# Kernel tuning notes

Hardware: AMD Instinct MI355X
Metric: run time of the kernel (lower is better)

The kernel has to match this reference:

```python
import jax, jax.numpy as jnp
import numpy as np

NUM_ROUTING = 3


def squash(t, axis=-1):
    # scale * t / ||t||, scale = ||t||^2 / (1 + ||t||^2)  (matches torch code exactly)
    norm = jnp.sum(t * t, axis=axis, keepdims=True)
    return (norm / (1.0 + norm)) * t / jnp.sqrt(norm)


def setup_inputs() -> dict:
    key = jax.random.key(0)
    k1, k2 = jax.random.split(key)
    x = jax.random.normal(k1, (512, 8, 1152), dtype=jnp.float32)      # [B, in_unit, in_channel]
    W = jax.random.normal(k2, (1, 1152, 10, 16, 8), dtype=jnp.float32)  # [1, C, U, unit_size, in_unit]
    return {"x": x, "W": W}


def reference(x, W):
    B = x.shape[0]
    # x.transpose(1,2): [B, C, I];  u_hat = W @ x  -> [B, C, U, O]  (O = unit_size)
    xt = jnp.transpose(x, (0, 2, 1))
    u_hat = jnp.einsum('cuoi,bci->bcuo', W[0], xt)
    # routing logits b_ij, shared across batch: [C, U]
    b = jnp.zeros(u_hat.shape[1:3], dtype=u_hat.dtype)
    v = None
    for _ in range(NUM_ROUTING):
        c = jax.nn.softmax(b, axis=1)                       # softmax over num_unit dim
        s = jnp.einsum('cu,bcuo->buo', c, u_hat)            # sum over in_channel
        v = squash(s, axis=-1)                              # squash over unit_size
        agree = jnp.einsum('bcuo,buo->cu', u_hat, v) / B    # mean over batch
        b = b + agree
    # torch returns v_j.squeeze(1) with trailing singleton -> [B, U, O, 1]
    return v[..., None]
```

## Files before the change

kernel.cpp:

```cpp
#include <hip/hip_runtime.h>
#include <math.h>

#define B_ 512
#define C_ 1152
#define U_ 10
#define O_ 16
#define I_ 8
#define K_ 9216
#define UO_ 160
#define NBLK 256
#define NTHR 256

typedef short bf16x8 __attribute__((ext_vector_type(8)));
typedef float f32x4 __attribute__((ext_vector_type(4)));
typedef unsigned short u16x8v __attribute__((ext_vector_type(8)));
typedef unsigned long long u64t;

__device__ __attribute__((aligned(16))) unsigned short g_xb2[B_*K_];
__device__ __attribute__((aligned(16))) unsigned short g_xT2[K_*B_];
__device__ __attribute__((aligned(16))) unsigned short g_Wc[3][C_*1280];
__device__ __attribute__((aligned(16))) unsigned g_vT32[2][UO_*B_/2];
__device__ float g_b[C_*U_];
__device__ unsigned g_gen;
__device__ unsigned g_arrive[NBLK];

__device__ __forceinline__ unsigned short f2bf(float f) {
    unsigned u = __builtin_bit_cast(unsigned, f);
    unsigned r = (u + 0x7FFFu + ((u >> 16) & 1u)) >> 16;
    return (unsigned short)r;
}

__device__ __forceinline__ void st_sys16(unsigned short* p, u16x8v v) {
    union { u16x8v v; u64t q[2]; } u; u.v = v;
    __hip_atomic_store((u64t*)p,     u.q[0], __ATOMIC_RELAXED, __HIP_MEMORY_SCOPE_SYSTEM);
    __hip_atomic_store(((u64t*)p)+1, u.q[1], __ATOMIC_RELAXED, __HIP_MEMORY_SCOPE_SYSTEM);
}

__global__ __launch_bounds__(256) void k_prep(const float* __restrict__ x,
                                              const float* __restrict__ W) {
    __shared__ unsigned short lds[32*256];
    int task = blockIdx.x, tid = threadIdx.x;
    if (task < 576) {
        int b0 = (task & 15) * 32;
        int c0 = (task >> 4) * 32;
        int li = tid >> 5, lc = tid & 31;
        for (int rep = 0; rep < 32; rep++) {
            float v = x[(b0+rep)*K_ + li*1152 + c0 + lc];
            lds[rep*256 + ((lc*8+li) ^ ((rep&31)<<3))] = f2bf(v);
        }
        __syncthreads();
        {
            int b = tid >> 3, part = tid & 7;
            int swz = (b&31) << 3;
            const u16x8v* lv = (const u16x8v*)lds;
            u16x8v* ov = (u16x8v*)(g_xb2 + (b0+b)*K_ + c0*8 + part*32);
            #pragma unroll
            for (int g = 0; g < 4; g++)
                ov[g] = lv[(b*256 + ((part*32 + g*8) ^ swz)) >> 3];
        }
        for (int p = 0; p < 8; p++) {
            int r = p*32 + (tid>>3);
            int bp = (tid&7)*4;
            ushort4 o;
            unsigned short* po = (unsigned short*)&o;
            #pragma unroll
            for (int q = 0; q < 4; q++) {
                int b = bp + q;
                po[q] = lds[b*256 + (r ^ ((b&31)<<3))];
            }
            *(ushort4*)(g_xT2 + (c0*8 + r)*B_ + b0 + bp) = o;
        }
    } else {
        int base = (task - 576) * 8192;
        for (int j = 0; j < 8; j++) {
            float4 v = *(const float4*)(W + base + j*1024 + tid*4);
            ushort4 o;
            o.x = f2bf(0.1f*v.x); o.y = f2bf(0.1f*v.y);
            o.z = f2bf(0.1f*v.z); o.w = f2bf(0.1f*v.w);
            *(ushort4*)(&g_Wc[0][0] + base + j*1024 + tid*4) = o;
        }
    }
}

union ShMem {
    float red[4][16][32];
    struct { float agg[2][U_]; float cws[2][U_]; } tb;
};

__device__ __forceinline__ void gbar(unsigned target) {
    __syncthreads();
    if (threadIdx.x == 0)
        __hip_atomic_store(&g_arrive[blockIdx.x], target,
                           __ATOMIC_RELAXED, __HIP_MEMORY_SCOPE_SYSTEM);
    if (blockIdx.x == 0) {
        long spins = 0;
        for (;;) {
            unsigned a = __hip_atomic_load(&g_arrive[threadIdx.x],
                                           __ATOMIC_RELAXED, __HIP_MEMORY_SCOPE_SYSTEM);
            if (__syncthreads_count((int)(a - target) >= 0) == NTHR) break;
            __builtin_amdgcn_s_sleep(4);
            if (++spins > (1L << 17)) break;
        }
        if (threadIdx.x == 0)
            __hip_atomic_store(&g_gen, target, __ATOMIC_RELAXED, __HIP_MEMORY_SCOPE_SYSTEM);
    }
    if (threadIdx.x == 0) {
        long spins = 0;
        while ((int)(__hip_atomic_load(&g_gen, __ATOMIC_RELAXED, __HIP_MEMORY_SCOPE_SYSTEM) - target) < 0) {
            __builtin_amdgcn_s_sleep(8);
            if (++spins > (1L << 18)) break;
        }
    }
    __syncthreads();
}

__device__ void ph_s(const unsigned short* __restrict__ Wcr, unsigned* vtw,
                     float* __restrict__ out, int bid, int tid, ShMem& sh) {
    if (bid < 160) {
        int lane = tid & 63, w = tid >> 6;
        int mt = bid & 31, nt = bid >> 5;
        int m0 = mt*16, n0 = nt*32;
        int ra = lane & 15, kq = (lane>>4)*8;
        const unsigned short* pa  = g_xb2 + (m0+ra)*K_ + w*2304 + kq;
        const unsigned short* pb0 = Wcr + (w*288 + (kq>>3))*1280 + (n0+ra)*8;
        const unsigned short* pb1 = pb0 + 128;
        f32x4 acc0 = {0.f,0.f,0.f,0.f};
        f32x4 acc1 = {0.f,0.f,0.f,0.f};
        #pragma unroll 6
        for (int s = 0; s < 72; s++) {
            bf16x8 a  = *(const bf16x8*)pa;
            bf16x8 b0 = *(const bf16x8*)pb0;
            bf16x8 b1 = *(const bf16x8*)pb1;
            acc0 = __builtin_amdgcn_mfma_f32_16x16x32_bf16(a, b0, acc0, 0, 0, 0);
            acc1 = __builtin_amdgcn_mfma_f32_16x16x32_bf16(a, b1, acc1, 0, 0, 0);
            pa += 32; pb0 += 5120; pb1 += 5120;
        }
        int row = (lane>>4)*4, col = lane & 15;
        #pragma unroll
        for (int r = 0; r < 4; r++) {
            sh.red[w][row+r][col]    = acc0[r];
            sh.red[w][row+r][col+16] = acc1[r];
        }
        __syncthreads();
        int bp = tid >> 5;
        int u  = (tid >> 4) & 1;
        int o  = tid & 15;
        int col2 = u*16 + o;
        float t0 = sh.red[0][2*bp][col2] + sh.red[1][2*bp][col2] + sh.red[2][2*bp][col2] + sh.red[3][2*bp][col2];
        float t1 = sh.red[0][2*bp+1][col2] + sh.red[1][2*bp+1][col2] + sh.red[2][2*bp+1][col2] + sh.red[3][2*bp+1][col2];
        float n0s = t0*t0, n1s = t1*t1;
        #pragma unroll
        for (int m = 1; m < 16; m <<= 1) {
            n0s += __shfl_xor(n0s, m);
            n1s += __shfl_xor(n1s, m);
        }
        float f0 = n0s / ((1.f + n0s) * sqrtf(n0s));
        float f1 = n1s / ((1.f + n1s) * sqrtf(n1s));
        float v0 = t0*f0, v1 = t1*f1;
        int ug = nt*2 + u;
        int bg = m0 + 2*bp;
        if (vtw) {
            unsigned pack = (unsigned)f2bf(v0) | ((unsigned)f2bf(v1) << 16);
            __hip_atomic_store(&vtw[((ug*16+o)*B_ + bg) >> 1], pack,
                               __ATOMIC_RELAXED, __HIP_MEMORY_SCOPE_SYSTEM);
        } else {
            out[(bg*10 + ug)*16 + o]       = v0;
            out[((bg+1)*10 + ug)*16 + o]   = v1;
        }
        __syncthreads();
    }
}

__device__ void ph_tb(const float* __restrict__ W, const unsigned* vtr,
                      unsigned short* Wcw, int first, int bid, int tid, ShMem& sh) {
    int lane = tid & 63, w = tid >> 6;
    const unsigned short* vT = (const unsigned short*)vtr;
    for (int task = bid; task < 576; task += NBLK) {
        int c0 = task * 2;
        int ra = lane & 15, kq = (lane>>4)*8;
        int ct = lane >> 5;
        int i0 = ((lane>>4) & 1) * 4;
        int o  = lane & 15;
        const unsigned short* pa0 = g_xT2 + (c0*8 + ra)*B_ + kq;
        for (int nt = w; nt < 5; nt += 4) {
            int n0 = nt*32;
            const unsigned short* pa  = pa0;
            const unsigned short* pb0 = vT + (n0+ra)*B_ + kq;
            const unsigned short* pb1 = pb0 + 16*B_;
            f32x4 acc0 = {0.f,0.f,0.f,0.f};
            f32x4 acc1 = {0.f,0.f,0.f,0.f};
            #pragma unroll 4
            for (int s = 0; s < 16; s++) {
                bf16x8 a  = *(const bf16x8*)pa;
                bf16x8 b0 = *(const bf16x8*)pb0;
                bf16x8 b1 = *(const bf16x8*)pb1;
                acc0 = __builtin_amdgcn_mfma_f32_16x16x32_bf16(a, b0, acc0, 0, 0, 0);
                acc1 = __builtin_amdgcn_mfma_f32_16x16x32_bf16(a, b1, acc1, 0, 0, 0);
                pa += 32; pb0 += 32; pb1 += 32;
            }
            const float* wr = W + (c0+ct)*1280;
            float4 wa = *(const float4*)(wr + (2*nt  )*128 + o*8 + i0);
            float4 wb = *(const float4*)(wr + (2*nt+1)*128 + o*8 + i0);
            float p0 = wa.x*acc0[0] + wa.y*acc0[1] + wa.z*acc0[2] + wa.w*acc0[3];
            float p1 = wb.x*acc1[0] + wb.y*acc1[1] + wb.z*acc1[2] + wb.w*acc1[3];
            #pragma unroll
            for (int m = 1; m < 32; m <<= 1) {
                p0 += __shfl_xor(p0, m);
                p1 += __shfl_xor(p1, m);
            }
            if ((lane & 31) == 0) {
                sh.tb.agg[ct][2*nt]   = p0 * (1.f/512.f);
                sh.tb.agg[ct][2*nt+1] = p1 * (1.f/512.f);
            }
        }
        __syncthreads();
        if (tid < 2) {
            int c = c0 + tid;
            float bv[U_];
            float mx = -3e38f;
            #pragma unroll
            for (int u = 0; u < U_; u++) {
                float v = sh.tb.agg[tid][u];
                if (!first) v += g_b[c*U_ + u];
                g_b[c*U_ + u] = v;
                bv[u] = v;
                mx = fmaxf(mx, v);
            }
            float sm = 0.f;
            #pragma unroll
            for (int u = 0; u < U_; u++) { bv[u] = expf(bv[u] - mx); sm += bv[u]; }
            float inv = 1.f/sm;
            #pragma unroll
            for (int u = 0; u < U_; u++) sh.tb.cws[tid][u] = bv[u]*inv;
        }
        __syncthreads();
        for (int e = tid*8; e < 2560; e += NTHR*8) {
            int ch  = (e >= 1280) ? 1 : 0;
            int off = e - ch*1280;
            int u   = off >> 7;
            float s = sh.tb.cws[ch][u];
            const float* wp = W + (c0+ch)*1280 + off;
            float4 a4 = *(const float4*)wp;
            float4 b4 = *(const float4*)(wp + 4);
            u16x8v ov;
            ov[0] = f2bf(a4.x*s); ov[1] = f2bf(a4.y*s); ov[2] = f2bf(a4.z*s); ov[3] = f2bf(a4.w*s);
            ov[4] = f2bf(b4.x*s); ov[5] = f2bf(b4.y*s); ov[6] = f2bf(b4.z*s); ov[7] = f2bf(b4.w*s);
            st_sys16(Wcw + (c0+ch)*1280 + off, ov);
        }
        __syncthreads();
    }
}

__global__ __launch_bounds__(NTHR) void k_mega(const float* __restrict__ W,
                                               float* __restrict__ out) {
    __shared__ ShMem sh;
    __shared__ unsigned sG0;
    int bid = blockIdx.x, tid = threadIdx.x;
    if (tid == 0)
        sG0 = __hip_atomic_load(&g_gen, __ATOMIC_RELAXED, __HIP_MEMORY_SCOPE_SYSTEM);
    __syncthreads();
    unsigned G0 = sG0;
    ph_s(&g_Wc[0][0], &g_vT32[0][0], out, bid, tid, sh);
    gbar(G0 + 1);
    ph_tb(W, &g_vT32[0][0], &g_Wc[1][0], 1, bid, tid, sh);
    gbar(G0 + 2);
    ph_s(&g_Wc[1][0], &g_vT32[1][0], out, bid, tid, sh);
    gbar(G0 + 3);
    ph_tb(W, &g_vT32[1][0], &g_Wc[2][0], 0, bid, tid, sh);
    gbar(G0 + 4);
    ph_s(&g_Wc[2][0], nullptr, out, bid, tid, sh);
}

extern "C" void kernel_launch(void* const* d_in, const int* in_sizes, int n_in,
                              void* d_out, int out_size, void* d_ws, size_t ws_size,
                              hipStream_t stream) {
    const float* x = (const float*)d_in[0];
    const float* W = (const float*)d_in[1];
    float* out = (float*)d_out;
    k_prep<<<dim3(756), dim3(256), 0, stream>>>(x, W);
    k_mega<<<dim3(NBLK), dim3(NTHR), 0, stream>>>(W, out);
}
```

Baseline: 145.3 us.

## Quadruple block size to split GEMM K across 16 waves and batch routing tasks

Raises threads per block from 256 to 1024 in the persistent megakernel. The s-phase GEMM now splits the K reduction across 16 waves instead of 4, giving each wave 18 MFMA steps instead of 72 and reducing the partial sums in a larger LDS array. The routing phase runs up to four channel-pair tasks at once per block, one per 256-thread group, instead of looping over them. This aims to shorten the serial latency chains and raise occupancy, at the cost of a wider LDS reduction, larger block-wide barriers, and idle threads in the squash epilogue. The grid barrier is also adjusted so only the first 256 threads poll arrival flags.

After: 123.9 us. 14.7% less time.

```diff
diff --git a/kernel.cpp b/kernel.cpp
--- a/kernel.cpp
+++ b/kernel.cpp
@@ -9,7 +9,7 @@
 #define K_ 9216
 #define UO_ 160
 #define NBLK 256
-#define NTHR 256
+#define NTHR 1024
 
 typedef short bf16x8 __attribute__((ext_vector_type(8)));
 typedef float f32x4 __attribute__((ext_vector_type(4)));
@@ -82,9 +82,10 @@
     }
 }
 
+struct TBsh { float agg[2][U_]; float cws[2][U_]; };
 union ShMem {
-    float red[4][16][32];
-    struct { float agg[2][U_]; float cws[2][U_]; } tb;
+    float red[16][16][32];
+    TBsh tb[4];
 };
 
 __device__ __forceinline__ void gbar(unsigned target) {
@@ -95,9 +96,13 @@
     if (blockIdx.x == 0) {
         long spins = 0;
         for (;;) {
-            unsigned a = __hip_atomic_load(&g_arrive[threadIdx.x],
-                                           __ATOMIC_RELAXED, __HIP_MEMORY_SCOPE_SYSTEM);
-            if (__syncthreads_count((int)(a - target) >= 0) == NTHR) break;
+            int ok = 1;
+            if (threadIdx.x < NBLK) {
+                unsigned a = __hip_atomic_load(&g_arrive[threadIdx.x],
+                                               __ATOMIC_RELAXED, __HIP_MEMORY_SCOPE_SYSTEM);
+                ok = (int)(a - target) >= 0;
+            }
+            if (__syncthreads_count(ok) == NTHR) break;
             __builtin_amdgcn_s_sleep(4);
             if (++spins > (1L << 17)) break;
         }
@@ -120,14 +125,14 @@
         int lane = tid & 63, w = tid >> 6;
         int mt = bid & 31, nt = bid >> 5;
         int m0 = mt*16, n0 = nt*32;
-        int ra = lane & 15, kq = (lane>>4)*8;
-        const unsigned short* pa  = g_xb2 + (m0+ra)*K_ + w*2304 + kq;
-        const unsigned short* pb0 = Wcr + (w*288 + (kq>>3))*1280 + (n0+ra)*8;
+        int ra = lane & 15;
+        const unsigned short* pa  = g_xb2 + (m0+ra)*K_ + w*576 + (lane>>4)*8;
+        const unsigned short* pb0 = Wcr + (w*72 + (lane>>4))*1280 + (n0+ra)*8;
         const unsigned short* pb1 = pb0 + 128;
         f32x4 acc0 = {0.f,0.f,0.f,0.f};
         f32x4 acc1 = {0.f,0.f,0.f,0.f};
         #pragma unroll 6
-        for (int s = 0; s < 72; s++) {
+        for (int s = 0; s < 18; s++) {
             bf16x8 a  = *(const bf16x8*)pa;
             bf16x8 b0 = *(const bf16x8*)pb0;
             bf16x8 b1 = *(const bf16x8*)pb1;
@@ -142,30 +147,36 @@
             sh.red[w][row+r][col+16] = acc1[r];
         }
         __syncthreads();
-        int bp = tid >> 5;
-        int u  = (tid >> 4) & 1;
-        int o  = tid & 15;
-        int col2 = u*16 + o;
-        float t0 = sh.red[0][2*bp][col2] + sh.red[1][2*bp][col2] + sh.red[2][2*bp][col2] + sh.red[3][2*bp][col2];
-        float t1 = sh.red[0][2*bp+1][col2] + sh.red[1][2*bp+1][col2] + sh.red[2][2*bp+1][col2] + sh.red[3][2*bp+1][col2];
-        float n0s = t0*t0, n1s = t1*t1;
-        #pragma unroll
-        for (int m = 1; m < 16; m <<= 1) {
-            n0s += __shfl_xor(n0s, m);
-            n1s += __shfl_xor(n1s, m);
-        }
-        float f0 = n0s / ((1.f + n0s) * sqrtf(n0s));
-        float f1 = n1s / ((1.f + n1s) * sqrtf(n1s));
-        float v0 = t0*f0, v1 = t1*f1;
-        int ug = nt*2 + u;
-        int bg = m0 + 2*bp;
-        if (vtw) {
-            unsigned pack = (unsigned)f2bf(v0) | ((unsigned)f2bf(v1) << 16);
-            __hip_atomic_store(&vtw[((ug*16+o)*B_ + bg) >> 1], pack,
-                               __ATOMIC_RELAXED, __HIP_MEMORY_SCOPE_SYSTEM);
-        } else {
-            out[(bg*10 + ug)*16 + o]       = v0;
-            out[((bg+1)*10 + ug)*16 + o]   = v1;
+        if (tid < 256) {
+            int bp = tid >> 5;
+            int u  = (tid >> 4) & 1;
+            int o  = tid & 15;
+            int col2 = u*16 + o;
+            float t0 = 0.f, t1 = 0.f;
+            #pragma unroll
+            for (int ww = 0; ww < 16; ww++) {
+                t0 += sh.red[ww][2*bp][col2];
+                t1 += sh.red[ww][2*bp+1][col2];
+            }
+            float n0s = t0*t0, n1s = t1*t1;
+            #pragma unroll
+            for (int m = 1; m < 16; m <<= 1) {
+                n0s += __shfl_xor(n0s, m);
+                n1s += __shfl_xor(n1s, m);
+            }
+            float f0 = n0s / ((1.f + n0s) * sqrtf(n0s));
+            float f1 = n1s / ((1.f + n1s) * sqrtf(n1s));
+            float v0 = t0*f0, v1 = t1*f1;
+            int ug = nt*2 + u;
+            int bg = m0 + 2*bp;
+            if (vtw) {
+                unsigned pack = (unsigned)f2bf(v0) | ((unsigned)f2bf(v1) << 16);
+                __hip_atomic_store(&vtw[((ug*16+o)*B_ + bg) >> 1], pack,
+                                   __ATOMIC_RELAXED, __HIP_MEMORY_SCOPE_SYSTEM);
+            } else {
+                out[(bg*10 + ug)*16 + o]       = v0;
+                out[((bg+1)*10 + ug)*16 + o]   = v1;
+            }
         }
         __syncthreads();
     }
@@ -173,16 +184,19 @@
 
 __device__ void ph_tb(const float* __restrict__ W, const unsigned* vtr,
                       unsigned short* Wcw, int first, int bid, int tid, ShMem& sh) {
-    int lane = tid & 63, w = tid >> 6;
+    int lane = tid & 63, lw = (tid >> 6) & 3, g = tid >> 8;
+    int ltid = tid & 255;
+    int t = bid + 256*g;
+    int valid = (t < 576);
     const unsigned short* vT = (const unsigned short*)vtr;
-    for (int task = bid; task < 576; task += NBLK) {
-        int c0 = task * 2;
-        int ra = lane & 15, kq = (lane>>4)*8;
-        int ct = lane >> 5;
-        int i0 = ((lane>>4) & 1) * 4;
-        int o  = lane & 15;
+    int c0 = t * 2;
+    int ra = lane & 15, kq = (lane>>4)*8;
+    int ct = lane >> 5;
+    int i0 = ((lane>>4) & 1) * 4;
+    int o  = lane & 15;
+    if (valid) {
         const unsigned short* pa0 = g_xT2 + (c0*8 + ra)*B_ + kq;
-        for (int nt = w; nt < 5; nt += 4) {
+        for (int nt = lw; nt < 5; nt += 4) {
             int n0 = nt*32;
             const unsigned short* pa  = pa0;
             const unsigned short* pb0 = vT + (n0+ra)*B_ + kq;
@@ -209,36 +223,38 @@
                 p1 += __shfl_xor(p1, m);
             }
             if ((lane & 31) == 0) {
-                sh.tb.agg[ct][2*nt]   = p0 * (1.f/512.f);
-                sh.tb.agg[ct][2*nt+1] = p1 * (1.f/512.f);
-            }
-        }
-        __syncthreads();
-        if (tid < 2) {
-            int c = c0 + tid;
-            float bv[U_];
-            float mx = -3e38f;
-            #pragma unroll
-            for (int u = 0; u < U_; u++) {
-                float v = sh.tb.agg[tid][u];
-                if (!first) v += g_b[c*U_ + u];
-                g_b[c*U_ + u] = v;
-                bv[u] = v;
-                mx = fmaxf(mx, v);
-            }
-            float sm = 0.f;
-            #pragma unroll
-            for (int u = 0; u < U_; u++) { bv[u] = expf(bv[u] - mx); sm += bv[u]; }
-            float inv = 1.f/sm;
-            #pragma unroll
-            for (int u = 0; u < U_; u++) sh.tb.cws[tid][u] = bv[u]*inv;
-        }
-        __syncthreads();
-        for (int e = tid*8; e < 2560; e += NTHR*8) {
+                sh.tb[g].agg[ct][2*nt]   = p0 * (1.f/512.f);
+                sh.tb[g].agg[ct][2*nt+1] = p1 * (1.f/512.f);
+            }
+        }
+    }
+    __syncthreads();
+    if (valid && ltid < 2) {
+        int c = c0 + ltid;
+        float bv[U_];
+        float mx = -3e38f;
+        #pragma unroll
+        for (int u = 0; u < U_; u++) {
+            float v = sh.tb[g].agg[ltid][u];
+            if (!first) v += g_b[c*U_ + u];
+            g_b[c*U_ + u] = v;
+            bv[u] = v;
+            mx = fmaxf(mx, v);
+        }
+        float sm = 0.f;
+        #pragma unroll
+        for (int u = 0; u < U_; u++) { bv[u] = expf(bv[u] - mx); sm += bv[u]; }
+        float inv = 1.f/sm;
+        #pragma unroll
+        for (int u = 0; u < U_; u++) sh.tb[g].cws[ltid][u] = bv[u]*inv;
+    }
+    __syncthreads();
+    if (valid) {
+        for (int e = ltid*8; e < 2560; e += 2048) {
             int ch  = (e >= 1280) ? 1 : 0;
             int off = e - ch*1280;
             int u   = off >> 7;
-            float s = sh.tb.cws[ch][u];
+            float s = sh.tb[g].cws[ch][u];
             const float* wp = W + (c0+ch)*1280 + off;
             float4 a4 = *(const float4*)wp;
             float4 b4 = *(const float4*)(wp + 4);
@@ -247,8 +263,8 @@
             ov[4] = f2bf(b4.x*s); ov[5] = f2bf(b4.y*s); ov[6] = f2bf(b4.z*s); ov[7] = f2bf(b4.w*s);
             st_sys16(Wcw + (c0+ch)*1280 + off, ov);
         }
-        __syncthreads();
-    }
+    }
+    __syncthreads();
 }
 
 __global__ __launch_bounds__(NTHR) void k_mega(const float* __restrict__ W,
```
